# Performance work log

Measured on AMD Instinct MI355X. Metric: run time of the kernel, lower is better.

## Reference

```python
import jax, jax.numpy as jnp
import numpy as np

N, E = 100000, 1600000
IN, T, H, C = 56, 16, 4, 16
HID, OUT = 64, 64
NEG_SLOPE = 0.2   # PyG GATConv default negative_slope
LN_EPS = 1e-5


def setup_inputs() -> dict:
    key = jax.random.key(0)
    k = jax.random.split(key, 12)
    g = lambda kk, shape: jax.random.normal(kk, shape, jnp.float32) * 0.1
    return {
        "x": jax.random.normal(k[0], (N, IN), jnp.float32),
        "temporal_features": jax.random.normal(k[1], (N, 1), jnp.float32),
        "edge_index": jax.random.randint(k[2], (2, E), 0, N, dtype=jnp.int32),
        "Wt": g(k[3], (1, T)), "bt": jnp.zeros((T,), jnp.float32),
        "W1": g(k[4], (IN + T, H * C)), "a_src1": g(k[5], (H, C)), "a_dst1": g(k[6], (H, C)),
        "b1": jnp.zeros((HID,), jnp.float32),
        "g1": jnp.ones((HID,), jnp.float32), "beta1": jnp.zeros((HID,), jnp.float32),
        "W2": g(k[7], (HID, H * C)), "a_src2": g(k[8], (H, C)), "a_dst2": g(k[9], (H, C)),
        "b2": jnp.zeros((OUT,), jnp.float32),
        "g2": jnp.ones((OUT,), jnp.float32), "beta2": jnp.zeros((OUT,), jnp.float32),
        "Wp1": g(k[10], (OUT, HID)), "bp1": jnp.zeros((HID,), jnp.float32),
        "Wp2": g(k[11], (HID, OUT)), "bp2": jnp.zeros((OUT,), jnp.float32),
    }


def _layer_norm(x, gamma, beta):
    mu = jnp.mean(x, -1, keepdims=True)
    var = jnp.var(x, -1, keepdims=True)
    return (x - mu) * jax.lax.rsqrt(var + LN_EPS) * gamma + beta


def _gat(x, src, dst, W, a_src, a_dst, bias, n):
    # linear transform per head (lin has no bias in PyG GATConv)
    h = (x @ W).reshape(n, H, C)                       # [N,H,C]
    s = jnp.einsum('nhc,hc->nh', h, a_src)             # att_src . h, per node
    d = jnp.einsum('nhc,hc->nh', h, a_dst)             # att_dst . h, per node
    e = jax.nn.leaky_relu(s[src] + d[dst], NEG_SLOPE)  # [Etot,H] per-edge logits
    # segment softmax over destination node (PyG softmax with +1e-16 denom)
    m = jax.ops.segment_max(e, dst, num_segments=n)
    e = jnp.exp(e - m[dst])
    z = jax.ops.segment_sum(e, dst, num_segments=n)
    alpha = e / (z[dst] + 1e-16)
    out = jax.ops.segment_sum(alpha[:, :, None] * h[src], dst, num_segments=n)
    return out.reshape(n, H * C) + bias


def reference(x, temporal_features, edge_index, Wt, bt, W1, a_src1, a_dst1, b1, g1, beta1,
              W2, a_src2, a_dst2, b2, g2, beta2, Wp1, bp1, Wp2, bp2):
    n = x.shape[0]
    t = jax.nn.relu(temporal_features @ Wt + bt)       # temporal encoder (dropout=identity, eval)
    xc = jnp.concatenate([x, t], axis=1)               # [N, 72]
    # add self-loops (PyG GATConv default add_self_loops=True)
    loop = jnp.arange(n, dtype=edge_index.dtype)
    src = jnp.concatenate([edge_index[0], loop])
    dst = jnp.concatenate([edge_index[1], loop])
    x1 = jax.nn.relu(_layer_norm(_gat(xc, src, dst, W1, a_src1, a_dst1, b1, n), g1, beta1))
    x2 = jax.nn.relu(_layer_norm(_gat(x1, src, dst, W2, a_src2, a_dst2, b2, n), g2, beta2))
    ge = jnp.mean(x2, axis=0)                          # batch=None -> global mean over nodes
    ge = jax.nn.relu(ge @ Wp1 + bp1) @ Wp2 + bp2       # global_pool MLP, then squeeze(0)
    return x2, ge
```

## Files before the change

### kernel.cpp

```cpp
#include <hip/hip_runtime.h>
#include <hip/hip_bf16.h>

#define NN    100000
#define EE    1600000
#define INF   56
#define TFEAT 16
#define K1    72

#define BUCKET_BITS 10
#define BUCKET_NODES (1 << BUCKET_BITS)
#define NB ((NN + BUCKET_NODES - 1) >> BUCKET_BITS)
#define BUCKET_CAP 20480
#define S1_EDGES 1024

__device__ __forceinline__ void fatomic_add(float* p, float v) {
    __hip_atomic_fetch_add(p, v, __ATOMIC_RELAXED, __HIP_MEMORY_SCOPE_AGENT);
}

__device__ __forceinline__ float lrelu(float v) { return v > 0.f ? v : 0.2f * v; }
__device__ __forceinline__ float bf2f(__hip_bfloat16 b) { return __bfloat162float(b); }
__device__ __forceinline__ float bfu2f(unsigned short u) {
    return __uint_as_float((unsigned)u << 16);
}
__device__ __forceinline__ unsigned short f2bfu(float f) {
    __hip_bfloat16 b = __float2bfloat16(f);
    return *reinterpret_cast<unsigned short*>(&b);
}

template <int K, bool TEMPORAL, bool IN_BF16>
__global__ void __launch_bounds__(256) feat_kernel(
    const void* __restrict__ xin_, const float* __restrict__ temp,
    const float* __restrict__ Wt, const float* __restrict__ bt,
    const float* __restrict__ W, const float* __restrict__ asrc,
    const float* __restrict__ adst,
    __hip_bfloat16* __restrict__ h, float* __restrict__ s, float* __restrict__ d)
{
    constexpr int WS = K + 4;
    __shared__ __align__(16) float Wl[64 * WS];
    __shared__ __align__(16) float xc[4 * WS];
    const int tid = threadIdx.x;
    const int n0 = blockIdx.x * 4;

    for (int i = tid; i < K * 64; i += 256) {
        int k = i >> 6, o = i & 63;
        Wl[o * WS + k] = W[i];
    }

    if (TEMPORAL) {
        const float* xin = (const float*)xin_;
        if (tid < 4 * INF) {
            int node = tid / INF, k = tid - node * INF;
            xc[node * WS + k] = xin[(n0 + node) * INF + k];
        }
        if (tid < 4 * TFEAT) {
            int node = tid >> 4, j = tid & 15;
            float tv = temp[n0 + node] * Wt[j] + bt[j];
            xc[node * WS + INF + j] = tv > 0.f ? tv : 0.f;
        }
    } else {
        int node = tid >> 6, k = tid & 63;
        if (IN_BF16) {
            const __hip_bfloat16* xin = (const __hip_bfloat16*)xin_;
            xc[node * WS + k] = bf2f(xin[(n0 + node) * 64 + k]);
        } else {
            const float* xin = (const float*)xin_;
            xc[node * WS + k] = xin[(n0 + node) * 64 + k];
        }
    }
    __syncthreads();

    const int node = tid >> 6, out = tid & 63;
    const float4* wrow = (const float4*)&Wl[out * WS];
    const float4* xrow = (const float4*)&xc[node * WS];
    float acc = 0.f;
#pragma unroll
    for (int k4 = 0; k4 < K / 4; k4++) {
        float4 wv = wrow[k4];
        float4 xv = xrow[k4];
        acc += wv.x * xv.x + wv.y * xv.y + wv.z * xv.z + wv.w * xv.w;
    }

    const int gn = n0 + node;
    h[gn * 64 + out] = __float2bfloat16(acc);

    const int head = out >> 4, c = out & 15;
    float vs = acc * asrc[head * 16 + c];
    float vd = acc * adst[head * 16 + c];
#pragma unroll
    for (int o = 8; o; o >>= 1) {
        vs += __shfl_down(vs, o, 16);
        vd += __shfl_down(vd, o, 16);
    }
    if (c == 0) { s[gn * 4 + head] = vs; d[gn * 4 + head] = vd; }
}

__global__ void __launch_bounds__(256) csr_s1_kernel(
    const int* __restrict__ esrc, const int* __restrict__ edst,
    int* __restrict__ bucketCnt, int* __restrict__ ebuf)
{
    __shared__ int hist[NB];
    __shared__ int base[NB];
    __shared__ int loff[NB];
    const int tid = threadIdx.x;
    const int e0 = blockIdx.x * S1_EDGES;

    for (int i = tid; i < NB; i += 256) { hist[i] = 0; loff[i] = 0; }
    __syncthreads();

    int val[4], bk[4];
#pragma unroll
    for (int t = 0; t < 4; t++) {
        int e = e0 + t * 256 + tid;
        if (e < EE) {
            int sn = esrc[e], dn = edst[e];
            int b = dn >> BUCKET_BITS;
            bk[t] = b;
            val[t] = ((dn & (BUCKET_NODES - 1)) << 17) | sn;
            atomicAdd(&hist[b], 1);
        } else bk[t] = -1;
    }
    __syncthreads();
    for (int i = tid; i < NB; i += 256)
        base[i] = hist[i] ? atomicAdd(&bucketCnt[i], hist[i]) : 0;
    __syncthreads();
#pragma unroll
    for (int t = 0; t < 4; t++) {
        if (bk[t] >= 0) {
            int pos = atomicAdd(&loff[bk[t]], 1);
            ebuf[bk[t] * BUCKET_CAP + base[bk[t]] + pos] = val[t];
        }
    }
}

__global__ void __launch_bounds__(256) csr_s2_kernel(
    const int* __restrict__ bucketCnt, const int* __restrict__ ebuf,
    int* __restrict__ deg, int* __restrict__ rowptr, int* __restrict__ csr_src)
{
    __shared__ int hist2[BUCKET_NODES];
    __shared__ int wsum[4];
    __shared__ int partial[256];
    const int b = blockIdx.x;
    const int tid = threadIdx.x;
    const int cnt = bucketCnt[b];
    const int nb0 = b << BUCKET_BITS;
    const int nnodes = min(BUCKET_NODES, NN - nb0);
    const int* seg = ebuf + b * BUCKET_CAP;

    partial[tid] = (tid < b) ? bucketCnt[tid] : 0;
    __syncthreads();
    for (int o = 128; o; o >>= 1) {
        if (tid < o) partial[tid] += partial[tid + o];
        __syncthreads();
    }
    const int cbase = partial[0];
    __syncthreads();

    for (int i = tid; i < BUCKET_NODES; i += 256) hist2[i] = 0;
    __syncthreads();
    for (int e = tid; e < cnt; e += 256) atomicAdd(&hist2[seg[e] >> 17], 1);
    __syncthreads();

    const int i0 = tid * 4;
    int h0 = hist2[i0], h1 = hist2[i0 + 1], h2 = hist2[i0 + 2], h3 = hist2[i0 + 3];
    int local = h0 + h1 + h2 + h3;
    int lane = tid & 63, wid = tid >> 6;
    int inc = local;
    for (int o = 1; o < 64; o <<= 1) {
        int u = __shfl_up(inc, o);
        if (lane >= o) inc += u;
    }
    if (lane == 63) wsum[wid] = inc;
    __syncthreads();
    int wbase = 0;
    for (int w = 0; w < wid; w++) wbase += wsum[w];
    int ebase = wbase + inc - local;
    __syncthreads();

    if (i0 < nnodes)     { deg[nb0 + i0]     = h0; rowptr[nb0 + i0]     = cbase + ebase; }
    if (i0 + 1 < nnodes) { deg[nb0 + i0 + 1] = h1; rowptr[nb0 + i0 + 1] = cbase + ebase + h0; }
    if (i0 + 2 < nnodes) { deg[nb0 + i0 + 2] = h2; rowptr[nb0 + i0 + 2] = cbase + ebase + h0 + h1; }
    if (i0 + 3 < nnodes) { deg[nb0 + i0 + 3] = h3; rowptr[nb0 + i0 + 3] = cbase + ebase + h0 + h1 + h2; }
    hist2[i0]     = ebase;
    hist2[i0 + 1] = ebase + h0;
    hist2[i0 + 2] = ebase + h0 + h1;
    hist2[i0 + 3] = ebase + h0 + h1 + h2;
    __syncthreads();

    for (int e = tid; e < cnt; e += 256) {
        int v = seg[e];
        int pos = atomicAdd(&hist2[v >> 17], 1);
        csr_src[cbase + pos] = v & 0x1FFFF;
    }
}

template <bool OUT_BF16>
__global__ void __launch_bounds__(256) agg_ln_kernel(
    const int* __restrict__ csr_src, const int* __restrict__ rowptr, const int* __restrict__ deg,
    const float* __restrict__ s, const float* __restrict__ d, const __hip_bfloat16* __restrict__ h,
    const float* __restrict__ bias, const float* __restrict__ gamma, const float* __restrict__ beta,
    void* __restrict__ out_)
{
    const int tid = threadIdx.x;
    const int wid = tid >> 6, lane = tid & 63;
    const int g = lane >> 4;
    const int li = lane & 15;
    const int head = li >> 2;
    const int c0 = li * 4;
    const int n = blockIdx.x * 16 + wid * 4 + g;

    const ushort4* hv4 = (const ushort4*)h;

    const float dv = d[n * 4 + head];
    float a0, a1, a2, a3, z;
    {
        float w = __expf(lrelu(s[n * 4 + head] + dv));
        ushort4 hv = hv4[n * 16 + li];
        a0 = w * bfu2f(hv.x); a1 = w * bfu2f(hv.y);
        a2 = w * bfu2f(hv.z); a3 = w * bfu2f(hv.w);
        z = w;
    }
    int j = rowptr[n];
    const int jend = j + deg[n];
    for (; j + 2 <= jend; j += 2) {
        int s0 = csr_src[j], s1 = csr_src[j + 1];
        float w0 = __expf(lrelu(s[s0 * 4 + head] + dv));
        float w1 = __expf(lrelu(s[s1 * 4 + head] + dv));
        ushort4 h0 = hv4[s0 * 16 + li];
        ushort4 h1 = hv4[s1 * 16 + li];
        a0 += w0 * bfu2f(h0.x) + w1 * bfu2f(h1.x);
        a1 += w0 * bfu2f(h0.y) + w1 * bfu2f(h1.y);
        a2 += w0 * bfu2f(h0.z) + w1 * bfu2f(h1.z);
        a3 += w0 * bfu2f(h0.w) + w1 * bfu2f(h1.w);
        z += w0 + w1;
    }
    if (j < jend) {
        int s0 = csr_src[j];
        float w0 = __expf(lrelu(s[s0 * 4 + head] + dv));
        ushort4 h0 = hv4[s0 * 16 + li];
        a0 += w0 * bfu2f(h0.x); a1 += w0 * bfu2f(h0.y);
        a2 += w0 * bfu2f(h0.z); a3 += w0 * bfu2f(h0.w);
        z += w0;
    }

    const float rz = 1.f / (z + 1e-16f);
    const float4 bv = *(const float4*)&bias[c0];
    float v0 = a0 * rz + bv.x, v1 = a1 * rz + bv.y;
    float v2 = a2 * rz + bv.z, v3 = a3 * rz + bv.w;

    float sum = (v0 + v1) + (v2 + v3);
    float sq  = (v0 * v0 + v1 * v1) + (v2 * v2 + v3 * v3);
#pragma unroll
    for (int o = 8; o; o >>= 1) { sum += __shfl_xor(sum, o); sq += __shfl_xor(sq, o); }
    float mu = sum * (1.f / 64.f);
    float var = sq * (1.f / 64.f) - mu * mu;
    float rs = rsqrtf(var + 1e-5f);
    const float4 gv = *(const float4*)&gamma[c0];
    const float4 bev = *(const float4*)&beta[c0];
    float y0 = (v0 - mu) * rs * gv.x + bev.x; y0 = y0 > 0.f ? y0 : 0.f;
    float y1 = (v1 - mu) * rs * gv.y + bev.y; y1 = y1 > 0.f ? y1 : 0.f;
    float y2 = (v2 - mu) * rs * gv.z + bev.z; y2 = y2 > 0.f ? y2 : 0.f;
    float y3 = (v3 - mu) * rs * gv.w + bev.w; y3 = y3 > 0.f ? y3 : 0.f;

    if (OUT_BF16) {
        ushort4 st = { f2bfu(y0), f2bfu(y1), f2bfu(y2), f2bfu(y3) };
        ((ushort4*)out_)[n * 16 + li] = st;
    } else {
        float4 st = { y0, y1, y2, y3 };
        ((float4*)out_)[n * 16 + li] = st;
    }
}

__global__ void __launch_bounds__(256) mean_kernel(const float* __restrict__ xin, float* __restrict__ meanacc) {
    __shared__ float sd[256];
    const int wid = threadIdx.x >> 6, c = threadIdx.x & 63;
    float csum = 0.f;
    for (int grp = blockIdx.x; grp < NN / 4; grp += 512) {
        int n = grp * 4 + wid;
        csum += xin[n * 64 + c];
    }
    sd[threadIdx.x] = csum;
    __syncthreads();
    if (threadIdx.x < 64) {
        fatomic_add(&meanacc[threadIdx.x],
                    sd[threadIdx.x] + sd[64 + threadIdx.x] + sd[128 + threadIdx.x] + sd[192 + threadIdx.x]);
    }
}

__global__ void __launch_bounds__(64) mlp_kernel(
    const float* __restrict__ meanacc,
    const float* __restrict__ Wp1, const float* __restrict__ bp1,
    const float* __restrict__ Wp2, const float* __restrict__ bp2,
    float* __restrict__ out)
{
    __shared__ float mean[64], hid[64];
    int t = threadIdx.x;
    mean[t] = meanacc[t] * (1.f / (float)NN);
    __syncthreads();
    float acc = bp1[t];
#pragma unroll
    for (int i = 0; i < 64; i++) acc += mean[i] * Wp1[i * 64 + t];
    hid[t] = acc > 0.f ? acc : 0.f;
    __syncthreads();
    float o = bp2[t];
#pragma unroll
    for (int i = 0; i < 64; i++) o += hid[i] * Wp2[i * 64 + t];
    out[NN * 64 + t] = o;
}

extern "C" void kernel_launch(void* const* d_in, const int* in_sizes, int n_in,
                              void* d_out, int out_size, void* d_ws, size_t ws_size,
                              hipStream_t stream) {
    const float* x    = (const float*)d_in[0];
    const float* temp = (const float*)d_in[1];
    const int*   ei   = (const int*)d_in[2];
    const float* Wt   = (const float*)d_in[3];
    const float* bt   = (const float*)d_in[4];
    const float* W1   = (const float*)d_in[5];
    const float* as1  = (const float*)d_in[6];
    const float* ad1  = (const float*)d_in[7];
    const float* b1   = (const float*)d_in[8];
    const float* g1   = (const float*)d_in[9];
    const float* be1  = (const float*)d_in[10];
    const float* W2   = (const float*)d_in[11];
    const float* as2  = (const float*)d_in[12];
    const float* ad2  = (const float*)d_in[13];
    const float* b2   = (const float*)d_in[14];
    const float* g2   = (const float*)d_in[15];
    const float* be2  = (const float*)d_in[16];
    const float* Wp1  = (const float*)d_in[17];
    const float* bp1  = (const float*)d_in[18];
    const float* Wp2  = (const float*)d_in[19];
    const float* bp2  = (const float*)d_in[20];

    float* out = (float*)d_out;

    char* w = (char*)d_ws;
    __hip_bfloat16* hb   = (__hip_bfloat16*)w;   w += (size_t)NN * 64 * 2;
    __hip_bfloat16* x1b  = (__hip_bfloat16*)w;   w += (size_t)NN * 64 * 2;
    float* sbuf    = (float*)w;                  w += (size_t)NN * 4 * 4;
    float* dbuf    = (float*)w;                  w += (size_t)NN * 4 * 4;
    float* meanacc = (float*)w;                  w += 256;
    int* bucketCnt = (int*)w;                    w += 512;
    int* deg       = (int*)w;                    w += (size_t)NN * 4;
    int* rowptr    = (int*)w;                    w += (size_t)NN * 4;
    int* csr_src   = (int*)w;                    w += (size_t)EE * 4;
    int* ebuf      = (int*)w;                    w += (size_t)NB * BUCKET_CAP * 4;

    const int* esrc = ei;
    const int* edst = ei + EE;

    hipMemsetAsync(bucketCnt, 0, 512, stream);
    hipMemsetAsync(meanacc, 0, 256, stream);

    csr_s1_kernel<<<(EE + S1_EDGES - 1) / S1_EDGES, 256, 0, stream>>>(esrc, edst, bucketCnt, ebuf);
    csr_s2_kernel<<<NB, 256, 0, stream>>>(bucketCnt, ebuf, deg, rowptr, csr_src);

    feat_kernel<K1, true, false><<<NN / 4, 256, 0, stream>>>(x, temp, Wt, bt, W1, as1, ad1, hb, sbuf, dbuf);
    agg_ln_kernel<true><<<NN / 16, 256, 0, stream>>>(csr_src, rowptr, deg, sbuf, dbuf, hb, b1, g1, be1, x1b);

    feat_kernel<64, false, true><<<NN / 4, 256, 0, stream>>>(x1b, nullptr, nullptr, nullptr, W2, as2, ad2, hb, sbuf, dbuf);
    agg_ln_kernel<false><<<NN / 16, 256, 0, stream>>>(csr_src, rowptr, deg, sbuf, dbuf, hb, b2, g2, be2, out);

    mean_kernel<<<512, 256, 0, stream>>>(out, meanacc);
    mlp_kernel<<<1, 64, 0, stream>>>(meanacc, Wp1, bp1, Wp2, bp2, out);
}
```

Before: 442.5 us.

## Register-tile feature GEMM: 64 nodes per block, 4x4 outputs per thread

The node feature transform now handles 64 nodes per block instead of 4, so the shared-memory weight load is spread over 16x more nodes. Each thread computes a 4-node by 4-output register tile with float4 weight and input loads, and writes bf16 results as ushort4. The attention score reductions use xor shuffles across 4 lanes. This cuts redundant weight staging and LDS traffic per FLOP, at the cost of more registers and fewer blocks, with bounds checks added for the partial last block.

```diff
diff --git a/kernel.cpp b/kernel.cpp
--- a/kernel.cpp
+++ b/kernel.cpp
@@ -35,63 +35,96 @@
     const float* __restrict__ adst,
     __hip_bfloat16* __restrict__ h, float* __restrict__ s, float* __restrict__ d)
 {
-    constexpr int WS = K + 4;
-    __shared__ __align__(16) float Wl[64 * WS];
-    __shared__ __align__(16) float xc[4 * WS];
+    constexpr int NPB = 64;
+    constexpr int WROW = 76;
+    __shared__ float4 Wl4[K * 16];
+    __shared__ __align__(16) float xc[NPB * WROW];
     const int tid = threadIdx.x;
-    const int n0 = blockIdx.x * 4;
-
-    for (int i = tid; i < K * 64; i += 256) {
-        int k = i >> 6, o = i & 63;
-        Wl[o * WS + k] = W[i];
-    }
+    const int n0 = blockIdx.x * NPB;
+
+    for (int i = tid; i < K * 16; i += 256)
+        Wl4[i] = *(const float4*)&W[(i >> 4) * 64 + (i & 15) * 4];
 
     if (TEMPORAL) {
         const float* xin = (const float*)xin_;
-        if (tid < 4 * INF) {
-            int node = tid / INF, k = tid - node * INF;
-            xc[node * WS + k] = xin[(n0 + node) * INF + k];
+        for (int i = tid; i < NPB * INF; i += 256) {
+            int n = i / INF, k = i - n * INF;
+            int gn = n0 + n;
+            xc[n * WROW + k] = (gn < NN) ? xin[gn * INF + k] : 0.f;
         }
-        if (tid < 4 * TFEAT) {
-            int node = tid >> 4, j = tid & 15;
-            float tv = temp[n0 + node] * Wt[j] + bt[j];
-            xc[node * WS + INF + j] = tv > 0.f ? tv : 0.f;
+        for (int i = tid; i < NPB * TFEAT; i += 256) {
+            int n = i >> 4, j = i & 15;
+            int gn = n0 + n;
+            float tv = (gn < NN) ? temp[gn] * Wt[j] + bt[j] : 0.f;
+            xc[n * WROW + INF + j] = tv > 0.f ? tv : 0.f;
         }
     } else {
-        int node = tid >> 6, k = tid & 63;
-        if (IN_BF16) {
-            const __hip_bfloat16* xin = (const __hip_bfloat16*)xin_;
-            xc[node * WS + k] = bf2f(xin[(n0 + node) * 64 + k]);
-        } else {
-            const float* xin = (const float*)xin_;
-            xc[node * WS + k] = xin[(n0 + node) * 64 + k];
+        const ushort4* xv4 = (const ushort4*)xin_;
+        for (int i = tid; i < NPB * 16; i += 256) {
+            int n = i >> 4, q = i & 15;
+            int gn = n0 + n;
+            float4 f = {0.f, 0.f, 0.f, 0.f};
+            if (gn < NN) {
+                ushort4 u = xv4[gn * 16 + q];
+                f.x = bfu2f(u.x); f.y = bfu2f(u.y); f.z = bfu2f(u.z); f.w = bfu2f(u.w);
+            }
+            *(float4*)&xc[n * WROW + q * 4] = f;
         }
     }
     __syncthreads();
 
-    const int node = tid >> 6, out = tid & 63;
-    const float4* wrow = (const float4*)&Wl[out * WS];
-    const float4* xrow = (const float4*)&xc[node * WS];
-    float acc = 0.f;
+    const int w = tid >> 6, lane = tid & 63;
+    const int li = lane & 15, gg = lane >> 4;
+    const int nb = w * 16 + gg * 4;
+
+    float4 a0 = {0,0,0,0}, a1 = {0,0,0,0}, a2 = {0,0,0,0}, a3 = {0,0,0,0};
+    const float4* xr0 = (const float4*)&xc[(nb + 0) * WROW];
+    const float4* xr1 = (const float4*)&xc[(nb + 1) * WROW];
+    const float4* xr2 = (const float4*)&xc[(nb + 2) * WROW];
+    const float4* xr3 = (const float4*)&xc[(nb + 3) * WROW];
+
+#define FMA4(A, XV) \
+    A.x += XV.x * w0.x + XV.y * w1.x + XV.z * w2.x + XV.w * w3.x; \
+    A.y += XV.x * w0.y + XV.y * w1.y + XV.z * w2.y + XV.w * w3.y; \
+    A.z += XV.x * w0.z + XV.y * w1.z + XV.z * w2.z + XV.w * w3.z; \
+    A.w += XV.x * w0.w + XV.y * w1.w + XV.z * w2.w + XV.w * w3.w;
+
 #pragma unroll
     for (int k4 = 0; k4 < K / 4; k4++) {
-        float4 wv = wrow[k4];
-        float4 xv = xrow[k4];
-        acc += wv.x * xv.x + wv.y * xv.y + wv.z * xv.z + wv.w * xv.w;
-    }
-
-    const int gn = n0 + node;
-    h[gn * 64 + out] = __float2bfloat16(acc);
-
-    const int head = out >> 4, c = out & 15;
-    float vs = acc * asrc[head * 16 + c];
-    float vd = acc * adst[head * 16 + c];
-#pragma unroll
-    for (int o = 8; o; o >>= 1) {
-        vs += __shfl_down(vs, o, 16);
-        vd += __shfl_down(vd, o, 16);
-    }
-    if (c == 0) { s[gn * 4 + head] = vs; d[gn * 4 + head] = vd; }
+        float4 w0 = Wl4[(4 * k4 + 0) * 16 + li];
+        float4 w1 = Wl4[(4 * k4 + 1) * 16 + li];
+        float4 w2 = Wl4[(4 * k4 + 2) * 16 + li];
+        float4 w3 = Wl4[(4 * k4 + 3) * 16 + li];
+        float4 x0 = xr0[k4], x1 = xr1[k4], x2 = xr2[k4], x3 = xr3[k4];
+        FMA4(a0, x0) FMA4(a1, x1) FMA4(a2, x2) FMA4(a3, x3)
+    }
+#undef FMA4
+
+    const int head = li >> 2;
+    const float4 as4 = *(const float4*)&asrc[li * 4];
+    const float4 ad4 = *(const float4*)&adst[li * 4];
+    float vs[4], vd[4];
+    float4* ap[4] = {&a0, &a1, &a2, &a3};
+#pragma unroll
+    for (int j = 0; j < 4; j++) {
+        float4 a = *ap[j];
+        vs[j] = a.x * as4.x + a.y * as4.y + a.z * as4.z + a.w * as4.w;
+        vd[j] = a.x * ad4.x + a.y * ad4.y + a.z * ad4.z + a.w * ad4.w;
+        vs[j] += __shfl_xor(vs[j], 1); vs[j] += __shfl_xor(vs[j], 2);
+        vd[j] += __shfl_xor(vd[j], 1); vd[j] += __shfl_xor(vd[j], 2);
+    }
+
+    ushort4* hv4 = (ushort4*)h;
+#pragma unroll
+    for (int j = 0; j < 4; j++) {
+        int gn = n0 + nb + j;
+        if (gn < NN) {
+            float4 a = *ap[j];
+            ushort4 st = { f2bfu(a.x), f2bfu(a.y), f2bfu(a.z), f2bfu(a.w) };
+            hv4[gn * 16 + li] = st;
+            if ((li & 3) == 0) { s[gn * 4 + head] = vs[j]; d[gn * 4 + head] = vd[j]; }
+        }
+    }
 }
 
 __global__ void __launch_bounds__(256) csr_s1_kernel(
@@ -355,10 +388,12 @@
     csr_s1_kernel<<<(EE + S1_EDGES - 1) / S1_EDGES, 256, 0, stream>>>(esrc, edst, bucketCnt, ebuf);
     csr_s2_kernel<<<NB, 256, 0, stream>>>(bucketCnt, ebuf, deg, rowptr, csr_src);
 
-    feat_kernel<K1, true, false><<<NN / 4, 256, 0, stream>>>(x, temp, Wt, bt, W1, as1, ad1, hb, sbuf, dbuf);
+    const int fgrid = (NN + 63) / 64;
+
+    feat_kernel<K1, true, false><<<fgrid, 256, 0, stream>>>(x, temp, Wt, bt, W1, as1, ad1, hb, sbuf, dbuf);
     agg_ln_kernel<true><<<NN / 16, 256, 0, stream>>>(csr_src, rowptr, deg, sbuf, dbuf, hb, b1, g1, be1, x1b);
 
-    feat_kernel<64, false, true><<<NN / 4, 256, 0, stream>>>(x1b, nullptr, nullptr, nullptr, W2, as2, ad2, hb, sbuf, dbuf);
+    feat_kernel<64, false, true><<<fgrid, 256, 0, stream>>>(x1b, nullptr, nullptr, nullptr, W2, as2, ad2, hb, sbuf, dbuf);
     agg_ln_kernel<false><<<NN / 16, 256, 0, stream>>>(csr_src, rowptr, deg, sbuf, dbuf, hb, b2, g2, be2, out);
 
     mean_kernel<<<512, 256, 0, stream>>>(out, meanacc);
```

New measurement: 369.4 us. 1.2x faster.
